# Kernel tuning notes

Hardware: AMD Instinct MI355X
Metric: run time of the kernel (lower is better)

Reference implementation:

```python
import jax, jax.numpy as jnp
import numpy as np

HEADS = 16
DIM_HEAD = 64
EPS = 1e-5

def layer_norm(x, g, b):
    mu = jnp.mean(x, axis=-1, keepdims=True)
    var = jnp.mean(jnp.square(x - mu), axis=-1, keepdims=True)
    return (x - mu) * jax.lax.rsqrt(var + EPS) * g + b

def setup_inputs() -> dict:
    key = jax.random.key(0)
    ks = jax.random.split(key, 8)
    b, n_t, n_a = 4, 1024, 1024
    text_dim, audio_dim = 1024, 1024
    inner = HEADS * DIM_HEAD  # 1024
    s_in = 1.0 / np.sqrt(audio_dim)
    return {
        "text": jax.random.normal(ks[0], (b, n_t, text_dim), jnp.float32),
        "audio": jax.random.normal(ks[1], (b, n_a, audio_dim), jnp.float32),
        "g_text": jnp.ones((text_dim,), jnp.float32),
        "b_text": jnp.zeros((text_dim,), jnp.float32),
        "g_audio": jnp.ones((audio_dim,), jnp.float32),
        "b_audio": jnp.zeros((audio_dim,), jnp.float32),
        "W_qk": jax.random.normal(ks[2], (audio_dim, inner), jnp.float32) * s_in,
        "W_v": jax.random.normal(ks[3], (text_dim, inner), jnp.float32) * s_in,
        "W_out": jax.random.normal(ks[4], (inner, audio_dim), jnp.float32) * s_in,
        "b_out": jnp.zeros((audio_dim,), jnp.float32),
        "W_th": jax.random.normal(ks[5], (HEADS, HEADS), jnp.float32) / np.sqrt(HEADS),
    }

def reference(text, audio, g_text, b_text, g_audio, b_audio, W_qk, W_v, W_out, b_out, W_th):
    b = audio.shape[0]
    scale = DIM_HEAD ** -0.5
    text = layer_norm(text, g_text, b_text)
    audio = layer_norm(audio, g_audio, b_audio)
    # projections; qk acts as query, v acts as BOTH key and value
    qk = (audio @ W_qk).reshape(b, -1, HEADS, DIM_HEAD).transpose(0, 2, 1, 3)  # b h i d
    v = (text @ W_v).reshape(b, -1, HEADS, DIM_HEAD).transpose(0, 2, 1, 3)    # b h j d
    sim = jnp.einsum('bhid,bhjd->bhij', qk, v) * scale
    attn = jax.nn.softmax(sim, axis=-1)
    # talking-heads: 1x1 conv over head dim == mixing matrix over h
    attn = jnp.einsum('hg,bgij->bhij', W_th, attn)
    out = jnp.einsum('bhij,bhjd->bhid', attn, v)
    out = out.transpose(0, 2, 1, 3).reshape(b, -1, HEADS * DIM_HEAD)
    return out @ W_out + b_out
```

## Files before the change

kernel.cpp:

```cpp
#include <hip/hip_runtime.h>

typedef unsigned short u16;
typedef __bf16 bf16x8 __attribute__((ext_vector_type(8)));
typedef float f32x4 __attribute__((ext_vector_type(4)));
typedef unsigned short u16x4 __attribute__((ext_vector_type(4)));

static __device__ __forceinline__ u16 f2bf(float f){
  __bf16 h = (__bf16)f;
  return __builtin_bit_cast(u16, h);
}

static __device__ __forceinline__ void gload16(const void* g, void* l){
  __builtin_amdgcn_global_load_lds(
      (const __attribute__((address_space(1))) unsigned int*)g,
      (__attribute__((address_space(3))) unsigned int*)l, 16, 0, 0);
}

#define MFMA(a,b,c) __builtin_amdgcn_mfma_f32_16x16x32_bf16(a,b,c,0,0,0)

__global__ __launch_bounds__(256) void ln_rows(const float* __restrict__ x,
    const float* __restrict__ g, const float* __restrict__ bta, u16* __restrict__ y)
{
  const int row = blockIdx.x;
  const int t = threadIdx.x;
  const float4 xv = ((const float4*)(x + (size_t)row*1024))[t];
  float s  = xv.x+xv.y+xv.z+xv.w;
  float sq = xv.x*xv.x+xv.y*xv.y+xv.z*xv.z+xv.w*xv.w;
  #pragma unroll
  for (int off=32; off; off>>=1){ s += __shfl_xor(s,off); sq += __shfl_xor(sq,off); }
  __shared__ float red[8];
  const int wid = t>>6, lane = t&63;
  if (lane==0){ red[wid]=s; red[4+wid]=sq; }
  __syncthreads();
  s  = red[0]+red[1]+red[2]+red[3];
  sq = red[4]+red[5]+red[6]+red[7];
  const float mu = s*(1.0f/1024.0f);
  float var = sq*(1.0f/1024.0f) - mu*mu;
  var = fmaxf(var, 0.0f);
  const float rs = rsqrtf(var + 1e-5f);
  const float4 gv = ((const float4*)g)[t];
  const float4 bv = ((const float4*)bta)[t];
  u16x4 o;
  o[0] = f2bf((xv.x-mu)*rs*gv.x + bv.x);
  o[1] = f2bf((xv.y-mu)*rs*gv.y + bv.y);
  o[2] = f2bf((xv.z-mu)*rs*gv.z + bv.z);
  o[3] = f2bf((xv.w-mu)*rs*gv.w + bv.w);
  ((u16x4*)(y + (size_t)row*1024))[t] = o;
}

__global__ __launch_bounds__(256) void transpose_w(const float* __restrict__ W, u16* __restrict__ WT)
{
  __shared__ float tile[32][33];
  const int tid = threadIdx.x;
  const int r0 = blockIdx.y*32, c0 = blockIdx.x*32;
  #pragma unroll
  for (int i=0;i<4;++i){
    int idx = i*256+tid; int r = idx>>5, c = idx&31;
    tile[r][c] = W[(size_t)(r0+r)*1024 + c0+c];
  }
  __syncthreads();
  #pragma unroll
  for (int i=0;i<4;++i){
    int idx = i*256+tid; int r = idx>>5, c = idx&31;
    WT[(size_t)(c0+r)*1024 + r0+c] = f2bf(tile[c][r]);
  }
}

__global__ __launch_bounds__(256) void transpose_v(const u16* __restrict__ V, u16* __restrict__ VT)
{
  __shared__ u16 tile[32][33];
  const int tid = threadIdx.x;
  const size_t base = (size_t)blockIdx.z * 1048576;
  const int r0 = blockIdx.y*32, c0 = blockIdx.x*32;
  #pragma unroll
  for (int i=0;i<4;++i){
    int idx = i*256+tid; int r = idx>>5, c = idx&31;
    tile[r][c] = V[base + (size_t)(r0+r)*1024 + c0+c];
  }
  __syncthreads();
  #pragma unroll
  for (int i=0;i<4;++i){
    int idx = i*256+tid; int r = idx>>5, c = idx&31;
    VT[base + (size_t)(c0+r)*1024 + r0+c] = tile[c][r];
  }
}

__global__ __launch_bounds__(256) void gemm_bt(const u16* __restrict__ A,
    const u16* __restrict__ Bt, u16* __restrict__ Cb, float* __restrict__ Cf,
    const float* __restrict__ bias, int outf)
{
  __shared__ u16 As[128][64];
  __shared__ u16 Bs[128][64];
  const int tid = threadIdx.x, lane = tid&63, wid = tid>>6;
  const int l15 = lane&15, l4 = lane>>4;
  const int m0 = blockIdx.y*128, n0 = blockIdx.x*128;
  const int wr = wid>>1, wc = wid&1;
  const int srow = wid*32 + (lane>>3);
  const int scol = (lane&7)*8;
  const u16* Ag = A  + (size_t)(m0+srow)*1024 + scol;
  const u16* Bg = Bt + (size_t)(n0+srow)*1024 + scol;
  f32x4 acc[4][4];
  #pragma unroll
  for (int mt=0;mt<4;++mt)
    #pragma unroll
    for (int nt=0;nt<4;++nt) acc[mt][nt] = f32x4{0,0,0,0};

  for (int kt=0; kt<16; ++kt){
    const int k0 = kt*64;
    #pragma unroll
    for (int c=0;c<4;++c){
      gload16(Ag + (size_t)c*8*1024 + k0, &As[wid*32 + c*8][0]);
      gload16(Bg + (size_t)c*8*1024 + k0, &Bs[wid*32 + c*8][0]);
    }
    __syncthreads();
    #pragma unroll
    for (int kk=0; kk<2; ++kk){
      bf16x8 af[4], bfv[4];
      #pragma unroll
      for (int mt=0;mt<4;++mt) af[mt]  = *(const bf16x8*)&As[wr*64+mt*16+l15][kk*32+8*l4];
      #pragma unroll
      for (int nt=0;nt<4;++nt) bfv[nt] = *(const bf16x8*)&Bs[wc*64+nt*16+l15][kk*32+8*l4];
      #pragma unroll
      for (int mt=0;mt<4;++mt)
        #pragma unroll
        for (int nt=0;nt<4;++nt)
          acc[mt][nt] = MFMA(af[mt], bfv[nt], acc[mt][nt]);
    }
    __syncthreads();
  }
  #pragma unroll
  for (int mt=0;mt<4;++mt)
    #pragma unroll
    for (int nt=0;nt<4;++nt)
      #pragma unroll
      for (int r=0;r<4;++r){
        const int row = m0 + wr*64+mt*16+l4*4+r;
        const int col = n0 + wc*64+nt*16+l15;
        if (outf) Cf[(size_t)row*1024+col] = acc[mt][nt][r] + bias[col];
        else      Cb[(size_t)row*1024+col] = f2bf(acc[mt][nt][r]);
      }
}

__global__ __launch_bounds__(256) void attn_stats(const u16* __restrict__ qk,
    const u16* __restrict__ v, float* __restrict__ m_arr, float* __restrict__ l_arr)
{
  const int lane = threadIdx.x & 63, wid = threadIdx.x >> 6;
  const int l15 = lane&15, l4 = lane>>4;
  const int b = blockIdx.z, g = blockIdx.y;
  const int i_base = blockIdx.x*64 + wid*16;
  const u16* qrow = qk + (size_t)(b*1024 + i_base + l15)*1024 + g*64 + 8*l4;
  const bf16x8 a0 = *(const bf16x8*)(qrow);
  const bf16x8 a1 = *(const bf16x8*)(qrow + 32);
  float mx[4] = {-1e30f,-1e30f,-1e30f,-1e30f};
  float sm[4] = {0.f,0.f,0.f,0.f};
  const u16* vbase = v + (size_t)(b*1024 + l15)*1024 + g*64 + 8*l4;
  for (int jt=0; jt<64; ++jt){
    const u16* vrow = vbase + (size_t)jt*16*1024;
    f32x4 c = {0,0,0,0};
    c = MFMA(a0, *(const bf16x8*)(vrow),      c);
    c = MFMA(a1, *(const bf16x8*)(vrow + 32), c);
    #pragma unroll
    for (int r=0;r<4;++r){
      const float s = c[r]*0.125f;
      const float nm = fmaxf(mx[r], s);
      sm[r] = sm[r]*__expf(mx[r]-nm) + __expf(s-nm);
      mx[r] = nm;
    }
  }
  #pragma unroll
  for (int r=0;r<4;++r){
    #pragma unroll
    for (int msk=1; msk<16; msk<<=1){
      const float om = __shfl_xor(mx[r], msk);
      const float os = __shfl_xor(sm[r], msk);
      const float nm = fmaxf(mx[r], om);
      sm[r] = sm[r]*__expf(mx[r]-nm) + os*__expf(om-nm);
      mx[r] = nm;
    }
  }
  if (l15 == 0){
    #pragma unroll
    for (int r=0;r<4;++r){
      const int i = i_base + l4*4 + r;
      const size_t idx = (size_t)(b*16+g)*1024 + i;
      m_arr[idx] = mx[r];
      l_arr[idx] = sm[r];
    }
  }
}

__global__ __launch_bounds__(512,4) void attn_mix_pv2(const u16* __restrict__ qk,
    const u16* __restrict__ v, const u16* __restrict__ vt,
    const float* __restrict__ m_arr, const float* __restrict__ l_arr,
    const float* __restrict__ Wth, float* __restrict__ Upart, int njt)
{
  __shared__ float wth[256];
  __shared__ float P[16][16][36];
  const int tid = threadIdx.x;
  const int lane = tid&63, wid = tid>>6;
  const int l15 = lane&15, l4 = lane>>4;
  const int b = blockIdx.y, z = blockIdx.z;
  const int i0 = blockIdx.x*16;
  const size_t bb = (size_t)b*1048576;
  if (tid < 256) wth[tid] = Wth[tid];

  float mxs[2][4], ils[2][4];
  bf16x8 aq[2][2];
  #pragma unroll
  for (int gg=0; gg<2; ++gg){
    const int g = 2*wid+gg;
    #pragma unroll
    for (int r=0;r<4;++r){
      const size_t idx = (size_t)(b*16+g)*1024 + i0 + 4*l4 + r;
      mxs[gg][r] = m_arr[idx];
      ils[gg][r] = 1.0f / l_arr[idx];
    }
    const u16* qrow = qk + bb + (size_t)(i0+l15)*1024 + g*64 + 8*l4;
    aq[gg][0] = *(const bf16x8*)qrow;
    aq[gg][1] = *(const bf16x8*)(qrow+32);
  }
  f32x4 acc[2][4];
  #pragma unroll
  for (int hh=0;hh<2;++hh)
    #pragma unroll
    for (int dt=0;dt<4;++dt) acc[hh][dt] = f32x4{0,0,0,0};

  for (int jt=0; jt<njt; ++jt){
    const int j0 = (z*njt + jt)*32;
    #pragma unroll
    for (int gg=0; gg<2; ++gg){
      const int g = 2*wid+gg;
      #pragma unroll
      for (int jh=0; jh<2; ++jh){
        const u16* vrow = v + bb + (size_t)(j0 + jh*16 + l15)*1024 + g*64 + 8*l4;
        f32x4 c = {0,0,0,0};
        c = MFMA(aq[gg][0], *(const bf16x8*)(vrow),      c);
        c = MFMA(aq[gg][1], *(const bf16x8*)(vrow + 32), c);
        #pragma unroll
        for (int r=0;r<4;++r)
          P[g][4*l4+r][jh*16+l15] = __expf(c[r]*0.125f - mxs[gg][r]) * ils[gg][r];
      }
    }
    __syncthreads();
    #pragma unroll
    for (int hh=0; hh<2; ++hh){
      const int h = 2*wid+hh;
      float bh[8];
      #pragma unroll
      for (int e=0;e<8;++e) bh[e] = 0.f;
      #pragma unroll
      for (int g2=0; g2<16; ++g2){
        const f32x4 p0 = *(const f32x4*)&P[g2][l15][8*l4];
        const f32x4 p1 = *(const f32x4*)&P[g2][l15][8*l4+4];
        const float w = wth[h*16+g2];
        #pragma unroll
        for (int e=0;e<4;++e){ bh[e] += w*p0[e]; bh[4+e] += w*p1[e]; }
      }
      bf16x8 pf;
      #pragma unroll
      for (int e=0;e<8;++e) pf[e] = (__bf16)bh[e];
      const u16* vtr = vt + bb + (size_t)(h*64 + l15)*1024 + j0 + 8*l4;
      #pragma unroll
      for (int dt=0; dt<4; ++dt)
        acc[hh][dt] = MFMA(pf, *(const bf16x8*)(vtr + (size_t)dt*16*1024), acc[hh][dt]);
    }
    __syncthreads();
  }
  #pragma unroll
  for (int hh=0; hh<2; ++hh)
    #pragma unroll
    for (int dt=0; dt<4; ++dt)
      #pragma unroll
      for (int r=0;r<4;++r){
        const size_t row = (size_t)z*4096 + b*1024 + i0 + 4*l4 + r;
        Upart[row*1024 + (2*wid+hh)*64 + dt*16 + l15] = acc[hh][dt][r];
      }
}

__global__ __launch_bounds__(256) void reduce_u(const float* __restrict__ Upart,
    u16* __restrict__ attn_o, int jc)
{
  const int row = blockIdx.x;
  const int t = threadIdx.x;
  f32x4 s = *(const f32x4*)(Upart + (size_t)row*1024 + 4*t);
  for (int z=1; z<jc; ++z)
    s += *(const f32x4*)(Upart + ((size_t)z*4096 + row)*1024 + 4*t);
  u16x4 o;
  #pragma unroll
  for (int e=0;e<4;++e) o[e] = f2bf(s[e]);
  *(u16x4*)(attn_o + (size_t)row*1024 + 4*t) = o;
}

extern "C" void kernel_launch(void* const* d_in, const int* in_sizes, int n_in,
                              void* d_out, int out_size, void* d_ws, size_t ws_size,
                              hipStream_t stream) {
  const float* text    = (const float*)d_in[0];
  const float* audio   = (const float*)d_in[1];
  const float* g_text  = (const float*)d_in[2];
  const float* b_text  = (const float*)d_in[3];
  const float* g_audio = (const float*)d_in[4];
  const float* b_audio = (const float*)d_in[5];
  const float* W_qk    = (const float*)d_in[6];
  const float* W_v     = (const float*)d_in[7];
  const float* W_out   = (const float*)d_in[8];
  const float* b_out   = (const float*)d_in[9];
  const float* W_th    = (const float*)d_in[10];

  char* ws = (char*)d_ws;
  const size_t MB = 1024*1024;
  u16* text_n  = (u16*)(ws + 0*MB);
  u16* audio_n = (u16*)(ws + 8*MB);
  u16* WqkT    = (u16*)(ws + 16*MB);
  u16* WvT     = (u16*)(ws + 18*MB);
  u16* WoutT   = (u16*)(ws + 20*MB);
  u16* qk      = (u16*)(ws + 22*MB);
  u16* v       = (u16*)(ws + 30*MB);
  u16* vt      = (u16*)(ws + 38*MB);
  float* m_arr = (float*)(ws + 16*MB);
  float* l_arr = (float*)(ws + 16*MB + 256*1024);

  const int jc = (ws_size >= 110*MB) ? 4 : 1;
  float* Upart;
  u16* attn_o;
  if (jc == 4){ Upart = (float*)(ws + 46*MB); attn_o = (u16*)(ws + 0*MB); }
  else        { Upart = (float*)(ws + 0*MB);  attn_o = (u16*)(ws + 46*MB); }

  transpose_w<<<dim3(32,32), 256, 0, stream>>>(W_qk,  WqkT);
  transpose_w<<<dim3(32,32), 256, 0, stream>>>(W_v,   WvT);
  transpose_w<<<dim3(32,32), 256, 0, stream>>>(W_out, WoutT);
  ln_rows<<<4096, 256, 0, stream>>>(text,  g_text,  b_text,  text_n);
  ln_rows<<<4096, 256, 0, stream>>>(audio, g_audio, b_audio, audio_n);
  gemm_bt<<<dim3(8,32), 256, 0, stream>>>(audio_n, WqkT, qk, nullptr, nullptr, 0);
  gemm_bt<<<dim3(8,32), 256, 0, stream>>>(text_n,  WvT,  v,  nullptr, nullptr, 0);
  transpose_v<<<dim3(32,32,4), 256, 0, stream>>>(v, vt);
  attn_stats<<<dim3(16,16,4), 256, 0, stream>>>(qk, v, m_arr, l_arr);
  attn_mix_pv2<<<dim3(64,4,jc), 512, 0, stream>>>(qk, v, vt, m_arr, l_arr, W_th, Upart, 32/jc);
  reduce_u<<<4096, 256, 0, stream>>>(Upart, attn_o, jc);
  gemm_bt<<<dim3(8,32), 256, 0, stream>>>(attn_o, WoutT, nullptr, (float*)d_out, b_out, 1);
}
```

Baseline: 319.6 us.

## Restructure talking-heads attention kernel: one head per wave, 32-row tiles, bf16 P

The mixing kernel now runs 16 waves per block, one head per wave, over 32 query rows instead of 16. Each V fragment loaded for QK^T is reused across both 16-row subtiles, and the softmax probability tile in LDS is stored as bf16 rather than fp32, which halves its LDS footprint and read traffic. The stats kernel now writes a single folded factor exp(-max)/sum per row, so the inner loop does one exp and one multiply instead of a subtract and a separate normalisation. In exchange, P loses precision before head mixing. The unnormalised exp and the separate exp(-max) factor can overflow or underflow when row maxima are large. The 1024-thread block with launch_bounds(1024,4) also puts strong register pressure on the kernel.

```diff
diff --git a/kernel.cpp b/kernel.cpp
--- a/kernel.cpp
+++ b/kernel.cpp
@@ -142,7 +142,7 @@
 }
 
 __global__ __launch_bounds__(256) void attn_stats(const u16* __restrict__ qk,
-    const u16* __restrict__ v, float* __restrict__ m_arr, float* __restrict__ l_arr)
+    const u16* __restrict__ v, float* __restrict__ k_arr)
 {
   const int lane = threadIdx.x & 63, wid = threadIdx.x >> 6;
   const int l15 = lane&15, l4 = lane>>4;
@@ -183,97 +183,94 @@
     for (int r=0;r<4;++r){
       const int i = i_base + l4*4 + r;
       const size_t idx = (size_t)(b*16+g)*1024 + i;
-      m_arr[idx] = mx[r];
-      l_arr[idx] = sm[r];
-    }
-  }
-}
-
-__global__ __launch_bounds__(512,4) void attn_mix_pv2(const u16* __restrict__ qk,
+      k_arr[idx] = __expf(-mx[r]) / sm[r];
+    }
+  }
+}
+
+__global__ __launch_bounds__(1024,4) void attn_mix_pv4(const u16* __restrict__ qk,
     const u16* __restrict__ v, const u16* __restrict__ vt,
-    const float* __restrict__ m_arr, const float* __restrict__ l_arr,
+    const float* __restrict__ k_arr,
     const float* __restrict__ Wth, float* __restrict__ Upart, int njt)
 {
   __shared__ float wth[256];
-  __shared__ float P[16][16][36];
+  __shared__ __align__(16) u16 P[16][32][40];
   const int tid = threadIdx.x;
   const int lane = tid&63, wid = tid>>6;
   const int l15 = lane&15, l4 = lane>>4;
   const int b = blockIdx.y, z = blockIdx.z;
-  const int i0 = blockIdx.x*16;
+  const int i0 = blockIdx.x*32;
   const size_t bb = (size_t)b*1048576;
   if (tid < 256) wth[tid] = Wth[tid];
 
-  float mxs[2][4], ils[2][4];
+  float kf[2][4];
+  #pragma unroll
+  for (int isub=0; isub<2; ++isub)
+    #pragma unroll
+    for (int r=0;r<4;++r)
+      kf[isub][r] = k_arr[(size_t)(b*16+wid)*1024 + i0 + isub*16 + 4*l4 + r];
+
   bf16x8 aq[2][2];
   #pragma unroll
-  for (int gg=0; gg<2; ++gg){
-    const int g = 2*wid+gg;
-    #pragma unroll
-    for (int r=0;r<4;++r){
-      const size_t idx = (size_t)(b*16+g)*1024 + i0 + 4*l4 + r;
-      mxs[gg][r] = m_arr[idx];
-      ils[gg][r] = 1.0f / l_arr[idx];
-    }
-    const u16* qrow = qk + bb + (size_t)(i0+l15)*1024 + g*64 + 8*l4;
-    aq[gg][0] = *(const bf16x8*)qrow;
-    aq[gg][1] = *(const bf16x8*)(qrow+32);
+  for (int isub=0; isub<2; ++isub){
+    const u16* qrow = qk + bb + (size_t)(i0 + isub*16 + l15)*1024 + wid*64 + 8*l4;
+    aq[isub][0] = *(const bf16x8*)qrow;
+    aq[isub][1] = *(const bf16x8*)(qrow+32);
   }
   f32x4 acc[2][4];
   #pragma unroll
-  for (int hh=0;hh<2;++hh)
-    #pragma unroll
-    for (int dt=0;dt<4;++dt) acc[hh][dt] = f32x4{0,0,0,0};
+  for (int isub=0;isub<2;++isub)
+    #pragma unroll
+    for (int dt=0;dt<4;++dt) acc[isub][dt] = f32x4{0,0,0,0};
 
   for (int jt=0; jt<njt; ++jt){
     const int j0 = (z*njt + jt)*32;
     #pragma unroll
-    for (int gg=0; gg<2; ++gg){
-      const int g = 2*wid+gg;
-      #pragma unroll
-      for (int jh=0; jh<2; ++jh){
-        const u16* vrow = v + bb + (size_t)(j0 + jh*16 + l15)*1024 + g*64 + 8*l4;
+    for (int jh=0; jh<2; ++jh){
+      const u16* vrow = v + bb + (size_t)(j0 + jh*16 + l15)*1024 + wid*64 + 8*l4;
+      const bf16x8 vf0 = *(const bf16x8*)(vrow);
+      const bf16x8 vf1 = *(const bf16x8*)(vrow + 32);
+      #pragma unroll
+      for (int isub=0; isub<2; ++isub){
         f32x4 c = {0,0,0,0};
-        c = MFMA(aq[gg][0], *(const bf16x8*)(vrow),      c);
-        c = MFMA(aq[gg][1], *(const bf16x8*)(vrow + 32), c);
+        c = MFMA(aq[isub][0], vf0, c);
+        c = MFMA(aq[isub][1], vf1, c);
         #pragma unroll
         for (int r=0;r<4;++r)
-          P[g][4*l4+r][jh*16+l15] = __expf(c[r]*0.125f - mxs[gg][r]) * ils[gg][r];
+          P[wid][isub*16 + 4*l4 + r][jh*16 + l15] = f2bf(__expf(c[r]*0.125f) * kf[isub][r]);
       }
     }
     __syncthreads();
     #pragma unroll
-    for (int hh=0; hh<2; ++hh){
-      const int h = 2*wid+hh;
+    for (int isub=0; isub<2; ++isub){
       float bh[8];
       #pragma unroll
       for (int e=0;e<8;++e) bh[e] = 0.f;
       #pragma unroll
       for (int g2=0; g2<16; ++g2){
-        const f32x4 p0 = *(const f32x4*)&P[g2][l15][8*l4];
-        const f32x4 p1 = *(const f32x4*)&P[g2][l15][8*l4+4];
-        const float w = wth[h*16+g2];
+        const bf16x8 p8 = *(const bf16x8*)&P[g2][isub*16 + l15][8*l4];
+        const float w = wth[wid*16+g2];
         #pragma unroll
-        for (int e=0;e<4;++e){ bh[e] += w*p0[e]; bh[4+e] += w*p1[e]; }
+        for (int e=0;e<8;++e) bh[e] += w*(float)p8[e];
       }
       bf16x8 pf;
       #pragma unroll
       for (int e=0;e<8;++e) pf[e] = (__bf16)bh[e];
-      const u16* vtr = vt + bb + (size_t)(h*64 + l15)*1024 + j0 + 8*l4;
+      const u16* vtr = vt + bb + (size_t)(wid*64 + l15)*1024 + j0 + 8*l4;
       #pragma unroll
       for (int dt=0; dt<4; ++dt)
-        acc[hh][dt] = MFMA(pf, *(const bf16x8*)(vtr + (size_t)dt*16*1024), acc[hh][dt]);
+        acc[isub][dt] = MFMA(pf, *(const bf16x8*)(vtr + (size_t)dt*16*1024), acc[isub][dt]);
     }
     __syncthreads();
   }
   #pragma unroll
-  for (int hh=0; hh<2; ++hh)
+  for (int isub=0; isub<2; ++isub)
     #pragma unroll
     for (int dt=0; dt<4; ++dt)
       #pragma unroll
       for (int r=0;r<4;++r){
-        const size_t row = (size_t)z*4096 + b*1024 + i0 + 4*l4 + r;
-        Upart[row*1024 + (2*wid+hh)*64 + dt*16 + l15] = acc[hh][dt][r];
+        const size_t row = (size_t)z*4096 + b*1024 + i0 + isub*16 + 4*l4 + r;
+        Upart[row*1024 + wid*64 + dt*16 + l15] = acc[isub][dt][r];
       }
 }
 
@@ -316,8 +313,7 @@
   u16* qk      = (u16*)(ws + 22*MB);
   u16* v       = (u16*)(ws + 30*MB);
   u16* vt      = (u16*)(ws + 38*MB);
-  float* m_arr = (float*)(ws + 16*MB);
-  float* l_arr = (float*)(ws + 16*MB + 256*1024);
+  float* k_arr = (float*)(ws + 16*MB);
 
   const int jc = (ws_size >= 110*MB) ? 4 : 1;
   float* Upart;
@@ -333,8 +329,8 @@
   gemm_bt<<<dim3(8,32), 256, 0, stream>>>(audio_n, WqkT, qk, nullptr, nullptr, 0);
   gemm_bt<<<dim3(8,32), 256, 0, stream>>>(text_n,  WvT,  v,  nullptr, nullptr, 0);
   transpose_v<<<dim3(32,32,4), 256, 0, stream>>>(v, vt);
-  attn_stats<<<dim3(16,16,4), 256, 0, stream>>>(qk, v, m_arr, l_arr);
-  attn_mix_pv2<<<dim3(64,4,jc), 512, 0, stream>>>(qk, v, vt, m_arr, l_arr, W_th, Upart, 32/jc);
+  attn_stats<<<dim3(16,16,4), 256, 0, stream>>>(qk, v, k_arr);
+  attn_mix_pv4<<<dim3(32,4,jc), 1024, 0, stream>>>(qk, v, vt, k_arr, W_th, Upart, 32/jc);
   reduce_u<<<4096, 256, 0, stream>>>(Upart, attn_o, jc);
   gemm_bt<<<dim3(8,32), 256, 0, stream>>>(attn_o, WoutT, nullptr, (float*)d_out, b_out, 1);
 }
```

New measurement: 374.5 us. +17.2%, slower.
